# Kernel tuning notes

Measured on AMD Instinct MI355X. Metric: run time of the kernel, lower is better.

The kernel has to match this reference:

```python
import jax, jax.numpy as jnp
import numpy as np

EPS = 1e-6
HEAD_DIM = 64
N_Q = 16
N_KV = 2

def setup_inputs() -> dict:
    key = jax.random.key(0)
    ks = jax.random.split(key, 4)
    H = 1024
    x = jax.random.normal(ks[0], (4, 8192, H), dtype=jnp.float32)
    ln_weight = jnp.zeros((H,), dtype=jnp.float32)  # Gemma param; scale is (1 + w)
    wq = jax.random.normal(ks[1], (H, HEAD_DIM * N_Q), dtype=jnp.float32) / np.sqrt(H)
    wk = jax.random.normal(ks[2], (H, HEAD_DIM * N_KV), dtype=jnp.float32) / np.sqrt(H)
    wv = jax.random.normal(ks[3], (H, HEAD_DIM * N_KV), dtype=jnp.float32) / np.sqrt(H)
    return {"x": x, "ln_weight": ln_weight, "wq": wq, "wk": wk, "wv": wv}

def gemma_rms_norm(x, w):
    xf = x.astype(jnp.float32)
    h = xf * jax.lax.rsqrt(jnp.mean(xf * xf, axis=-1, keepdims=True) + EPS)
    return (h * (1.0 + w.astype(jnp.float32))).astype(x.dtype)

def reference(x, ln_weight, wq, wk, wv):
    # Gemma RMSNorm prologue, then three linear projections (no bias).
    h = gemma_rms_norm(x, ln_weight)            # [B, S, H]
    q = jnp.einsum('bsh,hd->bsd', h, wq)        # [B, S, nq*d]
    k = jnp.einsum('bsh,hd->bsd', h, wk)        # [B, S, nkv*d]
    v = jnp.einsum('bsh,hd->bsd', h, wv)
    B, S = x.shape[0], x.shape[1]
    q = q.reshape(B, S, N_Q, HEAD_DIM)
    k = k.reshape(B, S, N_KV, HEAD_DIM)
    v = v.reshape(B, S, N_KV, HEAD_DIM)
    return (q, k, v)
```

## Files before the change

kernel.cpp:

```cpp
#include <hip/hip_runtime.h>
#include <hip/hip_bf16.h>

typedef __attribute__((ext_vector_type(4))) float f32x4;
typedef __attribute__((ext_vector_type(8))) short bf16x8;

#define H 1024
#define NTOT 1280
#define BM 256
#define BN 256
#define BK 64
#define NKT (H / BK)

static __device__ __forceinline__ unsigned short f2bf(float f) {
    __hip_bfloat16 b = __float2bfloat16(f);
    return __builtin_bit_cast(unsigned short, b);
}

#define GLOAD_LDS16(g, l)                                                     \
    __builtin_amdgcn_global_load_lds(                                         \
        (const __attribute__((address_space(1))) void*)(g),                   \
        (__attribute__((address_space(3))) void*)(l), 16, 0, 0)

__global__ __launch_bounds__(256) void k_rms(const float* __restrict__ x,
                                             __hip_bfloat16* __restrict__ h) {
    const int wave = threadIdx.x >> 6;
    const int lane = threadIdx.x & 63;
    const size_t row = (size_t)blockIdx.x * 4 + wave;

    const float4* xr = (const float4*)(x + row * H);
    float4 v[4];
    float ss = 0.f;
#pragma unroll
    for (int i = 0; i < 4; ++i) {
        v[i] = xr[lane + 64 * i];
        ss += v[i].x * v[i].x + v[i].y * v[i].y + v[i].z * v[i].z + v[i].w * v[i].w;
    }
#pragma unroll
    for (int o = 1; o < 64; o <<= 1) ss += __shfl_xor(ss, o);
    const float sc = rsqrtf(ss * (1.0f / H) + 1e-6f);

    ushort4* hr = (ushort4*)(h + row * H);
#pragma unroll
    for (int i = 0; i < 4; ++i) {
        ushort4 o4;
        o4.x = f2bf(v[i].x * sc);
        o4.y = f2bf(v[i].y * sc);
        o4.z = f2bf(v[i].z * sc);
        o4.w = f2bf(v[i].w * sc);
        hr[lane + 64 * i] = o4;
    }
}

__global__ __launch_bounds__(256) void k_wprep(const float* __restrict__ wq,
                                               const float* __restrict__ wk,
                                               const float* __restrict__ wv,
                                               const float* __restrict__ lnw,
                                               __hip_bfloat16* __restrict__ Bt) {
    const int idx = blockIdx.x * 256 + threadIdx.x;
    const int n = idx >> 10;
    const int k = idx & 1023;
    const float s = 1.0f + lnw[k];
    float w;
    if (n < 1024)       w = wq[k * 1024 + n];
    else if (n < 1152)  w = wk[k * 128 + (n - 1024)];
    else                w = wv[k * 128 + (n - 1152)];
    Bt[idx] = __float2bfloat16(s * w);
}

__global__ __launch_bounds__(512, 2) void k_gemm(const __hip_bfloat16* __restrict__ A,
                                                 const __hip_bfloat16* __restrict__ Bt,
                                                 float* __restrict__ out, int rows) {
    __shared__ __align__(16) char smem[131072];

    const int tid = threadIdx.x;
    const int lane = tid & 63;
    const int wid = tid >> 6;
    const int wm = wid >> 2;
    const int wn = wid & 3;

    const int nwg = gridDim.x;
    const int q8 = nwg >> 3, r8 = nwg & 7;
    const int xcd = blockIdx.x & 7, rank = blockIdx.x >> 3;
    const int wg = (xcd < r8 ? xcd * (q8 + 1) : r8 * (q8 + 1) + (xcd - r8) * q8) + rank;
    const int nt = wg % (NTOT / BN);
    const int mt = wg / (NTOT / BN);
    const size_t m0 = (size_t)mt * BM;

    const int cswz = ((tid & 7) * 16) ^ (((tid >> 3) & 7) << 4);
    const char* aG = (const char*)A + (m0 + (tid >> 3)) * (size_t)(H * 2) + cswz;
    const char* bG = (const char*)Bt + ((size_t)nt * BN + (tid >> 3)) * (size_t)(H * 2) + cswz;

#define STAGE(buf, kt)                                                        \
    {                                                                         \
        const char* as_ = aG + (size_t)(kt) * (BK * 2);                       \
        const char* bs_ = bG + (size_t)(kt) * (BK * 2);                       \
        char* ld_ = smem + (buf) * 65536 + tid * 16;                          \
        _Pragma("unroll") for (int j = 0; j < 4; ++j)                         \
            GLOAD_LDS16(as_ + (size_t)j * 64 * (H * 2), ld_ + j * 8192);      \
        _Pragma("unroll") for (int j = 0; j < 4; ++j)                         \
            GLOAD_LDS16(bs_ + (size_t)j * 64 * (H * 2), ld_ + 32768 + j * 8192); \
    }

    const int rowA = wm * 128 + (lane & 15);
    const int rowB = wn * 64 + (lane & 15);
    const int xm = (lane & 7) << 4;
    const int c0 = (((lane >> 4) * 16)) ^ xm;
    const int c1 = (64 + ((lane >> 4) * 16)) ^ xm;

    f32x4 acc[8][4] = {};

    STAGE(0, 0);
    STAGE(1, 1);

#define MFMA4x4(AF, BF, MIOFF)                                                \
    _Pragma("unroll") for (int mi = 0; mi < 4; ++mi)                          \
        _Pragma("unroll") for (int ni = 0; ni < 4; ++ni)                      \
            acc[(MIOFF) + mi][ni] = __builtin_amdgcn_mfma_f32_16x16x32_bf16(  \
                AF[mi], BF[ni], acc[(MIOFF) + mi][ni], 0, 0, 0);

#define TILE(cur, kt, DOSTAGE, VMSTR)                                         \
    {                                                                         \
        const char* aLb = smem + (cur) * 65536;                               \
        const char* bLb = aLb + 32768;                                        \
                                                                      \
        asm volatile("s_waitcnt vmcnt(" VMSTR ")" ::: "memory");              \
        __builtin_amdgcn_s_barrier();                                         \
        bf16x8 a0h0[4], b0[4];                                                \
        _Pragma("unroll") for (int mi = 0; mi < 4; ++mi)                      \
            a0h0[mi] = *(const bf16x8*)(aLb + (rowA + mi * 16) * 128 + c0);   \
        _Pragma("unroll") for (int ni = 0; ni < 4; ++ni)                      \
            b0[ni] = *(const bf16x8*)(bLb + (rowB + ni * 16) * 128 + c0);     \
        __builtin_amdgcn_s_barrier();                                         \
        asm volatile("s_waitcnt lgkmcnt(0)" ::: "memory");                    \
        __builtin_amdgcn_s_setprio(1);                                        \
        MFMA4x4(a0h0, b0, 0);                                                 \
        __builtin_amdgcn_s_setprio(0);                                        \
                                                                      \
        bf16x8 a0h1[4];                                                       \
        _Pragma("unroll") for (int mi = 0; mi < 4; ++mi)                      \
            a0h1[mi] = *(const bf16x8*)(aLb + (rowA + 64 + mi * 16) * 128 + c0); \
        __builtin_amdgcn_s_barrier();                                         \
        asm volatile("s_waitcnt lgkmcnt(0)" ::: "memory");                    \
        __builtin_amdgcn_s_setprio(1);                                        \
        MFMA4x4(a0h1, b0, 4);                                                 \
        __builtin_amdgcn_s_setprio(0);                                        \
                                                                      \
        bf16x8 a1h0[4], b1[4];                                                \
        _Pragma("unroll") for (int mi = 0; mi < 4; ++mi)                      \
            a1h0[mi] = *(const bf16x8*)(aLb + (rowA + mi * 16) * 128 + c1);   \
        _Pragma("unroll") for (int ni = 0; ni < 4; ++ni)                      \
            b1[ni] = *(const bf16x8*)(bLb + (rowB + ni * 16) * 128 + c1);     \
        __builtin_amdgcn_s_barrier();                                         \
        asm volatile("s_waitcnt lgkmcnt(0)" ::: "memory");                    \
        __builtin_amdgcn_s_setprio(1);                                        \
        MFMA4x4(a1h0, b1, 0);                                                 \
        __builtin_amdgcn_s_setprio(0);                                        \
                                                                      \
        bf16x8 a1h1[4];                                                       \
        _Pragma("unroll") for (int mi = 0; mi < 4; ++mi)                      \
            a1h1[mi] = *(const bf16x8*)(aLb + (rowA + 64 + mi * 16) * 128 + c1); \
        asm volatile("s_waitcnt lgkmcnt(0)" ::: "memory");                    \
        __builtin_amdgcn_s_barrier();                                         \
        if (DOSTAGE) STAGE(cur, (kt) + 2);                                    \
        __builtin_amdgcn_s_setprio(1);                                        \
        MFMA4x4(a1h1, b1, 4);                                                 \
        __builtin_amdgcn_s_setprio(0);                                        \
    }

    for (int kt = 0; kt < NKT - 2; kt += 2) {
        TILE(0, kt, true, "8");
        TILE(1, kt + 1, true, "8");
    }
    TILE(0, NKT - 2, false, "8");
    TILE(1, NKT - 1, false, "0");

    const size_t QSZ = (size_t)rows * 1024;
    const size_t KSZ = (size_t)rows * 128;
    const int colg0 = nt * BN + wn * 64;
    float* op;
    int ldc, cb0;
    if (colg0 < 1024)      { op = out;             ldc = 1024; cb0 = colg0; }
    else if (colg0 < 1152) { op = out + QSZ;       ldc = 128;  cb0 = colg0 - 1024; }
    else                   { op = out + QSZ + KSZ; ldc = 128;  cb0 = colg0 - 1152; }

    const size_t r0 = m0 + wm * 128 + ((lane >> 4) * 4);
    const int cc0 = cb0 + (lane & 15);
#pragma unroll
    for (int mi = 0; mi < 8; ++mi)
#pragma unroll
        for (int ni = 0; ni < 4; ++ni)
#pragma unroll
            for (int r = 0; r < 4; ++r)
                op[(r0 + mi * 16 + r) * (size_t)ldc + cc0 + ni * 16] = acc[mi][ni][r];
}

extern "C" void kernel_launch(void* const* d_in, const int* in_sizes, int n_in,
                              void* d_out, int out_size, void* d_ws, size_t ws_size,
                              hipStream_t stream) {
    const float* x   = (const float*)d_in[0];
    const float* lnw = (const float*)d_in[1];
    const float* wq  = (const float*)d_in[2];
    const float* wk  = (const float*)d_in[3];
    const float* wv  = (const float*)d_in[4];
    float* out = (float*)d_out;

    const int rows = in_sizes[0] / H;

    __hip_bfloat16* Bt = (__hip_bfloat16*)d_ws;
    __hip_bfloat16* h  = (__hip_bfloat16*)((char*)d_ws + (size_t)NTOT * H * 2);

    k_wprep<<<NTOT * H / 256, 256, 0, stream>>>(wq, wk, wv, lnw, Bt);
    k_rms<<<rows / 4, 256, 0, stream>>>(x, h);
    k_gemm<<<(rows / BM) * (NTOT / BN), 512, 0, stream>>>(h, Bt, out, rows);
}
```

Measured before the change: 156.6 us.

## Interleave global-to-LDS prefetch chunks across MFMA quadrants of each K tile

Restructures the GEMM main loop so each K tile is processed as four quadrant MFMA groups, each consuming both K halves at once. The next-tile global-to-LDS loads are split into chunks issued between quadrants, as soon as the rows they overwrite are no longer read, instead of all at once at the end. The vmcnt wait moves to the end of each tile, with an explicit wait and barrier after the prologue. This aims to overlap memory traffic with MFMA work and spread VMEM issue, at the cost of more barriers and more live fragment registers.

```diff
diff --git a/kernel.cpp b/kernel.cpp
--- a/kernel.cpp
+++ b/kernel.cpp
@@ -90,16 +90,12 @@
     const char* aG = (const char*)A + (m0 + (tid >> 3)) * (size_t)(H * 2) + cswz;
     const char* bG = (const char*)Bt + ((size_t)nt * BN + (tid >> 3)) * (size_t)(H * 2) + cswz;
 
-#define STAGE(buf, kt)                                                        \
-    {                                                                         \
-        const char* as_ = aG + (size_t)(kt) * (BK * 2);                       \
-        const char* bs_ = bG + (size_t)(kt) * (BK * 2);                       \
-        char* ld_ = smem + (buf) * 65536 + tid * 16;                          \
-        _Pragma("unroll") for (int j = 0; j < 4; ++j)                         \
-            GLOAD_LDS16(as_ + (size_t)j * 64 * (H * 2), ld_ + j * 8192);      \
-        _Pragma("unroll") for (int j = 0; j < 4; ++j)                         \
-            GLOAD_LDS16(bs_ + (size_t)j * 64 * (H * 2), ld_ + 32768 + j * 8192); \
-    }
+#define STAGE_A(buf, kt, q)                                                   \
+    GLOAD_LDS16(aG + (size_t)(kt) * (BK * 2) + (size_t)(q) * 64 * (H * 2),    \
+                smem + (buf) * 65536 + (q) * 8192 + tid * 16)
+#define STAGE_B(buf, kt, q)                                                   \
+    GLOAD_LDS16(bG + (size_t)(kt) * (BK * 2) + (size_t)(q) * 64 * (H * 2),    \
+                smem + (buf) * 65536 + 32768 + (q) * 8192 + tid * 16)
 
     const int rowA = wm * 128 + (lane & 15);
     const int rowB = wn * 64 + (lane & 15);
@@ -109,70 +105,88 @@
 
     f32x4 acc[8][4] = {};
 
-    STAGE(0, 0);
-    STAGE(1, 1);
-
-#define MFMA4x4(AF, BF, MIOFF)                                                \
+#pragma unroll
+    for (int q = 0; q < 4; ++q) { STAGE_A(0, 0, q); STAGE_B(0, 0, q); }
+#pragma unroll
+    for (int q = 0; q < 4; ++q) { STAGE_A(1, 1, q); STAGE_B(1, 1, q); }
+    asm volatile("s_waitcnt vmcnt(8)" ::: "memory");
+    __builtin_amdgcn_s_barrier();
+
+#define MFMA16(AK0, AK1, BK0, BK1, MIOFF, NIOFF)                              \
     _Pragma("unroll") for (int mi = 0; mi < 4; ++mi)                          \
-        _Pragma("unroll") for (int ni = 0; ni < 4; ++ni)                      \
-            acc[(MIOFF) + mi][ni] = __builtin_amdgcn_mfma_f32_16x16x32_bf16(  \
-                AF[mi], BF[ni], acc[(MIOFF) + mi][ni], 0, 0, 0);
+        _Pragma("unroll") for (int ni = 0; ni < 2; ++ni)                      \
+            acc[(MIOFF) + mi][(NIOFF) + ni] =                                 \
+                __builtin_amdgcn_mfma_f32_16x16x32_bf16(                      \
+                    AK0[mi], BK0[ni], acc[(MIOFF) + mi][(NIOFF) + ni], 0, 0, 0); \
+    _Pragma("unroll") for (int mi = 0; mi < 4; ++mi)                          \
+        _Pragma("unroll") for (int ni = 0; ni < 2; ++ni)                      \
+            acc[(MIOFF) + mi][(NIOFF) + ni] =                                 \
+                __builtin_amdgcn_mfma_f32_16x16x32_bf16(                      \
+                    AK1[mi], BK1[ni], acc[(MIOFF) + mi][(NIOFF) + ni], 0, 0, 0);
 
 #define TILE(cur, kt, DOSTAGE, VMSTR)                                         \
     {                                                                         \
         const char* aLb = smem + (cur) * 65536;                               \
         const char* bLb = aLb + 32768;                                        \
-                                                                      \
+                                            \
+        bf16x8 a0k0[4], a0k1[4], b0k0[2], b0k1[2];                            \
+        _Pragma("unroll") for (int mi = 0; mi < 4; ++mi) {                    \
+            a0k0[mi] = *(const bf16x8*)(aLb + (rowA + mi * 16) * 128 + c0);   \
+            a0k1[mi] = *(const bf16x8*)(aLb + (rowA + mi * 16) * 128 + c1);   \
+        }                                                                     \
+        _Pragma("unroll") for (int ni = 0; ni < 2; ++ni) {                    \
+            b0k0[ni] = *(const bf16x8*)(bLb + (rowB + ni * 16) * 128 + c0);   \
+            b0k1[ni] = *(const bf16x8*)(bLb + (rowB + ni * 16) * 128 + c1);   \
+        }                                                                     \
+        asm volatile("s_waitcnt lgkmcnt(8)" ::: "memory");                    \
+        __builtin_amdgcn_s_barrier();                                         \
+        asm volatile("s_waitcnt lgkmcnt(0)" ::: "memory");                    \
+        __builtin_amdgcn_s_setprio(1);                                        \
+        MFMA16(a0k0, a0k1, b0k0, b0k1, 0, 0);                                 \
+        __builtin_amdgcn_s_setprio(0);                                        \
+        __builtin_amdgcn_s_barrier();                                         \
+                \
+        if (DOSTAGE) { STAGE_A(cur, (kt) + 2, 0); STAGE_A(cur, (kt) + 2, 2); } \
+        bf16x8 b1k0[2], b1k1[2];                                              \
+        _Pragma("unroll") for (int ni = 0; ni < 2; ++ni) {                    \
+            b1k0[ni] = *(const bf16x8*)(bLb + (rowB + 32 + ni * 16) * 128 + c0); \
+            b1k1[ni] = *(const bf16x8*)(bLb + (rowB + 32 + ni * 16) * 128 + c1); \
+        }                                                                     \
+        __builtin_amdgcn_s_barrier();                                         \
+        asm volatile("s_waitcnt lgkmcnt(0)" ::: "memory");                    \
+        __builtin_amdgcn_s_setprio(1);                                        \
+        MFMA16(a0k0, a0k1, b1k0, b1k1, 0, 2);                                 \
+        __builtin_amdgcn_s_setprio(0);                                        \
+        __builtin_amdgcn_s_barrier();                                         \
+                       \
+        if (DOSTAGE) { STAGE_B(cur, (kt) + 2, 0); STAGE_B(cur, (kt) + 2, 1); } \
+        bf16x8 a1k0[4], a1k1[4];                                              \
+        _Pragma("unroll") for (int mi = 0; mi < 4; ++mi) {                    \
+            a1k0[mi] = *(const bf16x8*)(aLb + (rowA + 64 + mi * 16) * 128 + c0); \
+            a1k1[mi] = *(const bf16x8*)(aLb + (rowA + 64 + mi * 16) * 128 + c1); \
+        }                                                                     \
+        __builtin_amdgcn_s_barrier();                                         \
+        asm volatile("s_waitcnt lgkmcnt(0)" ::: "memory");                    \
+        __builtin_amdgcn_s_setprio(1);                                        \
+        MFMA16(a1k0, a1k1, b0k0, b0k1, 4, 0);                                 \
+        __builtin_amdgcn_s_setprio(0);                                        \
+        __builtin_amdgcn_s_barrier();                                         \
+                \
+        if (DOSTAGE) { STAGE_A(cur, (kt) + 2, 1); STAGE_A(cur, (kt) + 2, 3);  \
+                       STAGE_B(cur, (kt) + 2, 2); STAGE_B(cur, (kt) + 2, 3); } \
+        __builtin_amdgcn_s_setprio(1);                                        \
+        MFMA16(a1k0, a1k1, b1k0, b1k1, 4, 2);                                 \
+        __builtin_amdgcn_s_setprio(0);                                        \
         asm volatile("s_waitcnt vmcnt(" VMSTR ")" ::: "memory");              \
         __builtin_amdgcn_s_barrier();                                         \
-        bf16x8 a0h0[4], b0[4];                                                \
-        _Pragma("unroll") for (int mi = 0; mi < 4; ++mi)                      \
-            a0h0[mi] = *(const bf16x8*)(aLb + (rowA + mi * 16) * 128 + c0);   \
-        _Pragma("unroll") for (int ni = 0; ni < 4; ++ni)                      \
-            b0[ni] = *(const bf16x8*)(bLb + (rowB + ni * 16) * 128 + c0);     \
-        __builtin_amdgcn_s_barrier();                                         \
-        asm volatile("s_waitcnt lgkmcnt(0)" ::: "memory");                    \
-        __builtin_amdgcn_s_setprio(1);                                        \
-        MFMA4x4(a0h0, b0, 0);                                                 \
-        __builtin_amdgcn_s_setprio(0);                                        \
-                                                                      \
-        bf16x8 a0h1[4];                                                       \
-        _Pragma("unroll") for (int mi = 0; mi < 4; ++mi)                      \
-            a0h1[mi] = *(const bf16x8*)(aLb + (rowA + 64 + mi * 16) * 128 + c0); \
-        __builtin_amdgcn_s_barrier();                                         \
-        asm volatile("s_waitcnt lgkmcnt(0)" ::: "memory");                    \
-        __builtin_amdgcn_s_setprio(1);                                        \
-        MFMA4x4(a0h1, b0, 4);                                                 \
-        __builtin_amdgcn_s_setprio(0);                                        \
-                                                                      \
-        bf16x8 a1h0[4], b1[4];                                                \
-        _Pragma("unroll") for (int mi = 0; mi < 4; ++mi)                      \
-            a1h0[mi] = *(const bf16x8*)(aLb + (rowA + mi * 16) * 128 + c1);   \
-        _Pragma("unroll") for (int ni = 0; ni < 4; ++ni)                      \
-            b1[ni] = *(const bf16x8*)(bLb + (rowB + ni * 16) * 128 + c1);     \
-        __builtin_amdgcn_s_barrier();                                         \
-        asm volatile("s_waitcnt lgkmcnt(0)" ::: "memory");                    \
-        __builtin_amdgcn_s_setprio(1);                                        \
-        MFMA4x4(a1h0, b1, 0);                                                 \
-        __builtin_amdgcn_s_setprio(0);                                        \
-                                                                      \
-        bf16x8 a1h1[4];                                                       \
-        _Pragma("unroll") for (int mi = 0; mi < 4; ++mi)                      \
-            a1h1[mi] = *(const bf16x8*)(aLb + (rowA + 64 + mi * 16) * 128 + c1); \
-        asm volatile("s_waitcnt lgkmcnt(0)" ::: "memory");                    \
-        __builtin_amdgcn_s_barrier();                                         \
-        if (DOSTAGE) STAGE(cur, (kt) + 2);                                    \
-        __builtin_amdgcn_s_setprio(1);                                        \
-        MFMA4x4(a1h1, b1, 4);                                                 \
-        __builtin_amdgcn_s_setprio(0);                                        \
     }
 
     for (int kt = 0; kt < NKT - 2; kt += 2) {
-        TILE(0, kt, true, "8");
-        TILE(1, kt + 1, true, "8");
-    }
-    TILE(0, NKT - 2, false, "8");
-    TILE(1, NKT - 1, false, "0");
+        TILE(0, kt, 1, "8");
+        TILE(1, kt + 1, 1, "8");
+    }
+    TILE(0, NKT - 2, 0, "0");
+    TILE(1, NKT - 1, 0, "0");
 
     const size_t QSZ = (size_t)rows * 1024;
     const size_t KSZ = (size_t)rows * 128;
```

New measurement: 154.8 us. About the same (-1.2%).
